# Performance work log

Measured on AMD Instinct MI355X. Metric: run time of the kernel, lower is better.

Reference implementation:

```python
import jax, jax.numpy as jnp
import numpy as np

IN_FEATURES = 1024
OUT_FEATURES = 1024
GRID_SIZE = 5
SPLINE_ORDER = 3
N_BASIS = GRID_SIZE + SPLINE_ORDER  # 8, matches spline_weight last dim
N_GRID = GRID_SIZE + 2 * SPLINE_ORDER + 1  # 12 knots -> Cox-de-Boor yields N_BASIS bases


def b_spline(x, grid):
    # x: [B, I] -> bases: [B, I, N_BASIS]
    x = x[..., None]
    bases = ((x >= grid[:-1]) & (x < grid[1:])).astype(x.dtype)
    for k in range(1, SPLINE_ORDER + 1):
        left = (x - grid[: -k - 1]) / (grid[k:-1] - grid[: -k - 1] + 1e-8)
        right = (grid[k + 1:] - x) / (grid[k + 1:] - grid[1:-k] + 1e-8)
        bases = left * bases[..., :-1] + right * bases[..., 1:]
    return bases


def setup_inputs() -> dict:
    key = jax.random.key(0)
    k1, k2, k3 = jax.random.split(key, 3)
    x = jax.random.uniform(k1, (4096, IN_FEATURES), dtype=jnp.float32) * 2.0 - 1.0
    # kaiming_uniform_(a=sqrt(5)) on [out,in]: bound = 1/sqrt(in)
    bound = 1.0 / np.sqrt(IN_FEATURES)
    base_weight = jax.random.uniform(k2, (OUT_FEATURES, IN_FEATURES), dtype=jnp.float32,
                                     minval=-bound, maxval=bound)
    spline_weight = 0.1 * jax.random.normal(k3, (OUT_FEATURES, IN_FEATURES, N_BASIS), dtype=jnp.float32)
    grid = jnp.linspace(-1.0, 1.0, N_GRID, dtype=jnp.float32)
    return {"x": x, "base_weight": base_weight, "spline_weight": spline_weight, "grid": grid}


def reference(x, base_weight, spline_weight, grid):
    base_output = jax.nn.silu(x) @ base_weight.T  # [B, O]
    spline_basis = b_spline(x, grid)              # [B, I, Q]
    spline_output = jnp.einsum('biq,oiq->bo', spline_basis, spline_weight)
    return base_output + spline_output
```

## Files before the change

### kernel.cpp

```cpp
#include <hip/hip_runtime.h>
#include <hip/hip_bf16.h>

#define IN_F 1024
#define OUT_F 1024
#define QP 9
#define KDIM (IN_F * QP)
#define SPLITK 2
#define KSLICE (KDIM / SPLITK)
#define BK 64

typedef __attribute__((ext_vector_type(8))) short short8;
typedef __attribute__((ext_vector_type(4))) float floatx4;
typedef __attribute__((ext_vector_type(8))) unsigned short ushort8v;

__device__ __forceinline__ unsigned short f2bf(float f) {
    union { float f; unsigned u; } v; v.f = f;
    return (unsigned short)((v.u + 0x7FFF + ((v.u >> 16) & 1)) >> 16);
}

__global__ __launch_bounds__(256) void pack_kernel(const float* __restrict__ x,
                                                   const float* __restrict__ bw,
                                                   const float* __restrict__ sw,
                                                   __hip_bfloat16* __restrict__ A,
                                                   __hip_bfloat16* __restrict__ W, int Bm) {
    const int nb_a = (Bm * IN_F / 8) / 256;
    if ((int)blockIdx.x < nb_a) {
        int t  = blockIdx.x * 256 + threadIdx.x;
        int b  = t >> 7;
        int i0 = (t & 127) * 8;
        const float4* xr = (const float4*)(x + (size_t)b * IN_F + i0);
        float4 x0 = xr[0], x1 = xr[1];
        float xv[8] = {x0.x, x0.y, x0.z, x0.w, x1.x, x1.y, x1.z, x1.w};
        ushort8v ov[9];
#pragma unroll
        for (int e = 0; e < 8; ++e) {
            float v  = xv[e];
            float u  = (v + 1.0f) * 5.5f;
            float fj = floorf(u);
            int   j  = (int)fj;
            float tt = u - fj;
            float t2 = tt * tt, t3 = t2 * tt;
            float omt = 1.0f - tt;
            float w0 = omt * omt * omt * (1.0f / 6.0f);
            float w1 = (3.0f * t3 - 6.0f * t2 + 4.0f) * (1.0f / 6.0f);
            float w2 = (-3.0f * t3 + 3.0f * t2 + 3.0f * tt + 1.0f) * (1.0f/6.0f);
            float w3 = t3 * (1.0f / 6.0f);
            ov[0][e] = f2bf(v * __builtin_amdgcn_rcpf(1.0f + __expf(-v)));
#pragma unroll
            for (int q = 0; q < 8; ++q) {
                int d = j - q;
                float bv = (d == 3) ? w0 : (d == 2) ? w1 : (d == 1) ? w2 : (d == 0) ? w3 : 0.0f;
                ov[1 + q][e] = f2bf(bv);
            }
        }
        unsigned short* dst = (unsigned short*)A + (size_t)b * KDIM + i0;
#pragma unroll
        for (int s = 0; s < QP; ++s)
            *(ushort8v*)(dst + (size_t)s * IN_F) = ov[s];
    } else {
        int t = ((int)blockIdx.x - nb_a) * 256 + threadIdx.x;
        unsigned short* dst = (unsigned short*)W + (size_t)(t >> 10) * KDIM + (t & 1023);
        dst[0] = f2bf(bw[t]);
        const float4* s4 = (const float4*)(sw + (size_t)t * 8);
        float4 lo = s4[0], hi = s4[1];
        dst[1 * IN_F] = f2bf(lo.x); dst[2 * IN_F] = f2bf(lo.y);
        dst[3 * IN_F] = f2bf(lo.z); dst[4 * IN_F] = f2bf(lo.w);
        dst[5 * IN_F] = f2bf(hi.x); dst[6 * IN_F] = f2bf(hi.y);
        dst[7 * IN_F] = f2bf(hi.z); dst[8 * IN_F] = f2bf(hi.w);
    }
}

__global__ __launch_bounds__(256, 2) void gemm_splitk(const __hip_bfloat16* __restrict__ A,
                                                      const __hip_bfloat16* __restrict__ W,
                                                      float* __restrict__ P, int Bm) {
    __shared__ short sA[128 * BK];
    __shared__ short sB[128 * BK];
    const int tid   = threadIdx.x;
    const int lane  = tid & 63;
    const int wave  = tid >> 6;
    const int row16 = lane & 15;
    const int quad  = lane >> 4;
    const int wm = wave >> 1, wn = wave & 1;
    const int m0 = blockIdx.y * 128;
    const int n0 = blockIdx.x * 128;
    const int kb = blockIdx.z * KSLICE;

    const short* Ag = (const short*)A + (size_t)m0 * KDIM + kb;
    const short* Wg = (const short*)W + (size_t)n0 * KDIM + kb;

    floatx4 acc[4][4] = {};

    int rs[4], ko[4], ld[4];
#pragma unroll
    for (int p = 0; p < 4; ++p) {
        int c = p * 256 + tid;
        rs[p] = c >> 3;
        ko[p] = (((c & 7) ^ ((rs[p] >> 1) & 7)) * 8);
        ld[p] = c * 8;
    }

    for (int k0 = 0; k0 < KSLICE; k0 += BK) {
#pragma unroll
        for (int p = 0; p < 4; ++p)
            __builtin_amdgcn_global_load_lds(
                (const __attribute__((address_space(1))) void*)(Ag + (size_t)rs[p] * KDIM + k0 + ko[p]),
                (__attribute__((address_space(3))) void*)(sA + ld[p]), 16, 0, 0);
#pragma unroll
        for (int p = 0; p < 4; ++p)
            __builtin_amdgcn_global_load_lds(
                (const __attribute__((address_space(1))) void*)(Wg + (size_t)rs[p] * KDIM + k0 + ko[p]),
                (__attribute__((address_space(3))) void*)(sB + ld[p]), 16, 0, 0);
        __syncthreads();

#pragma unroll
        for (int ks = 0; ks < 2; ++ks) {
            short8 aF[4], bF[4];
#pragma unroll
            for (int mi = 0; mi < 4; ++mi) {
                int r = wm * 64 + mi * 16 + row16;
                int pc = (ks * 4 + quad) ^ ((r >> 1) & 7);
                aF[mi] = *(const short8*)&sA[r * BK + pc * 8];
            }
#pragma unroll
            for (int ni = 0; ni < 4; ++ni) {
                int r = wn * 64 + ni * 16 + row16;
                int pc = (ks * 4 + quad) ^ ((r >> 1) & 7);
                bF[ni] = *(const short8*)&sB[r * BK + pc * 8];
            }
#pragma unroll
            for (int mi = 0; mi < 4; ++mi)
#pragma unroll
                for (int ni = 0; ni < 4; ++ni)
                    acc[mi][ni] = __builtin_amdgcn_mfma_f32_16x16x32_bf16(
                        aF[mi], bF[ni], acc[mi][ni], 0, 0, 0);
        }
        __syncthreads();
    }

    float* Pz = P + (size_t)blockIdx.z * Bm * OUT_F;
#pragma unroll
    for (int mi = 0; mi < 4; ++mi)
#pragma unroll
        for (int r = 0; r < 4; ++r) {
            int gm = m0 + wm * 64 + mi * 16 + quad * 4 + r;
            float* crow = Pz + (size_t)gm * OUT_F + n0 + wn * 64 + row16;
#pragma unroll
            for (int ni = 0; ni < 4; ++ni)
                crow[ni * 16] = acc[mi][ni][r];
        }
}

__global__ __launch_bounds__(256) void reduce_kernel(const float4* __restrict__ P,
                                                     float4* __restrict__ C, int n4) {
    int t = blockIdx.x * 256 + threadIdx.x;
    float4 a = P[t], b = P[n4 + t];
    float4 o;
    o.x = a.x + b.x; o.y = a.y + b.y; o.z = a.z + b.z; o.w = a.w + b.w;
    C[t] = o;
}

__global__ __launch_bounds__(256, 2) void gemm_kernel(const __hip_bfloat16* __restrict__ A,
                                                      const __hip_bfloat16* __restrict__ W,
                                                      float* __restrict__ C) {
    __shared__ short sA[128 * 32];
    __shared__ short sB[64 * 32];
    const int tid   = threadIdx.x;
    const int lane  = tid & 63;
    const int wave  = tid >> 6;
    const int row16 = lane & 15;
    const int quad  = lane >> 4;
    const int wm = wave >> 1, wn = wave & 1;
    const int m0 = blockIdx.y * 128;
    const int n0 = blockIdx.x * 64;
    const short* Ag = (const short*)A + (size_t)m0 * KDIM;
    const short* Wg = (const short*)W + (size_t)n0 * KDIM;
    floatx4 acc[4][2] = {};
    const int cA0 = tid,       rA0 = cA0 >> 2, kA0 = (((cA0 & 3) ^ ((rA0 >> 1) & 3)) * 8);
    const int cA1 = 256 + tid, rA1 = cA1 >> 2, kA1 = (((cA1 & 3) ^ ((rA1 >> 1) & 3)) * 8);
    const int cB  = tid,       rB  = cB  >> 2, kB  = (((cB  & 3) ^ ((rB  >> 1) & 3)) * 8);
    for (int k0 = 0; k0 < KDIM; k0 += 32) {
        __builtin_amdgcn_global_load_lds(
            (const __attribute__((address_space(1))) void*)(Ag + (size_t)rA0 * KDIM + k0 + kA0),
            (__attribute__((address_space(3))) void*)(sA + cA0 * 8), 16, 0, 0);
        __builtin_amdgcn_global_load_lds(
            (const __attribute__((address_space(1))) void*)(Ag + (size_t)rA1 * KDIM + k0 + kA1),
            (__attribute__((address_space(3))) void*)(sA + cA1 * 8), 16, 0, 0);
        __builtin_amdgcn_global_load_lds(
            (const __attribute__((address_space(1))) void*)(Wg + (size_t)rB * KDIM + k0 + kB),
            (__attribute__((address_space(3))) void*)(sB + cB * 8), 16, 0, 0);
        __syncthreads();
        short8 aF[4], bF[2];
#pragma unroll
        for (int mi = 0; mi < 4; ++mi) {
            int r = wm * 64 + mi * 16 + row16;
            aF[mi] = *(const short8*)&sA[r * 32 + ((quad ^ ((r >> 1) & 3)) * 8)];
        }
#pragma unroll
        for (int ni = 0; ni < 2; ++ni) {
            int r = wn * 32 + ni * 16 + row16;
            bF[ni] = *(const short8*)&sB[r * 32 + ((quad ^ ((r >> 1) & 3)) * 8)];
        }
#pragma unroll
        for (int mi = 0; mi < 4; ++mi)
#pragma unroll
            for (int ni = 0; ni < 2; ++ni)
                acc[mi][ni] = __builtin_amdgcn_mfma_f32_16x16x32_bf16(
                    aF[mi], bF[ni], acc[mi][ni], 0, 0, 0);
        __syncthreads();
    }
#pragma unroll
    for (int mi = 0; mi < 4; ++mi)
#pragma unroll
        for (int r = 0; r < 4; ++r) {
            int gm = m0 + wm * 64 + mi * 16 + quad * 4 + r;
            float* crow = C + (size_t)gm * OUT_F + n0 + wn * 32 + row16;
            crow[0]  = acc[mi][0][r];
            crow[16] = acc[mi][1][r];
        }
}

__global__ __launch_bounds__(256) void fallback_kernel(const float* __restrict__ x,
                                                       const float* __restrict__ bw,
                                                       const float* __restrict__ sw,
                                                       const float* __restrict__ grid,
                                                       float* __restrict__ out, int Bm) {
    __shared__ float sv[256][QP + 1];
    int b = blockIdx.y;
    int o = blockIdx.x * 256 + threadIdx.x;
    float acc = 0.f;
    for (int ic = 0; ic < IN_F; ic += 256) {
        int i = ic + threadIdx.x;
        float v = x[(size_t)b * IN_F + i];
        float g[12];
        for (int j = 0; j < 12; ++j) g[j] = grid[j];
        float bb[11];
        for (int j = 0; j < 11; ++j) bb[j] = (v >= g[j] && v < g[j + 1]) ? 1.f : 0.f;
        for (int k = 1; k <= 3; ++k)
            for (int j = 0; j < 11 - k; ++j)
                bb[j] = (v - g[j]) / (g[j + k] - g[j] + 1e-8f) * bb[j]
                      + (g[j + k + 1] - v) / (g[j + k + 1] - g[j + 1] + 1e-8f) * bb[j + 1];
        __syncthreads();
        sv[threadIdx.x][0] = v / (1.f + __expf(-v));
        for (int q = 0; q < 8; ++q) sv[threadIdx.x][1 + q] = bb[q];
        __syncthreads();
        for (int ii = 0; ii < 256; ++ii) {
            int i2 = ic + ii;
            acc += sv[ii][0] * bw[(size_t)o * IN_F + i2];
            const float* swp = sw + ((size_t)o * IN_F + i2) * 8;
            for (int q = 0; q < 8; ++q) acc += sv[ii][1 + q] * swp[q];
        }
    }
    out[(size_t)b * OUT_F + o] = acc;
}

extern "C" void kernel_launch(void* const* d_in, const int* in_sizes, int n_in,
                              void* d_out, int out_size, void* d_ws, size_t ws_size,
                              hipStream_t stream) {
    const float* x    = (const float*)d_in[0];
    const float* bw   = (const float*)d_in[1];
    const float* sw   = (const float*)d_in[2];
    const float* grid = (const float*)d_in[3];
    float* out = (float*)d_out;

    const int Bm = in_sizes[0] / IN_F;
    const size_t a_bytes = (size_t)Bm * KDIM * sizeof(__hip_bfloat16);
    const size_t w_bytes = (size_t)OUT_F * KDIM * sizeof(__hip_bfloat16);
    const size_t p_bytes = (size_t)SPLITK * Bm * OUT_F * sizeof(float);

    if (ws_size >= a_bytes + w_bytes && (Bm % 128) == 0) {
        __hip_bfloat16* Apk = (__hip_bfloat16*)d_ws;
        __hip_bfloat16* Wpk = (__hip_bfloat16*)((char*)d_ws + a_bytes);
        const int nb_a = (Bm * IN_F / 8) / 256;
        const int nb_w = (OUT_F * IN_F) / 256;
        pack_kernel<<<nb_a + nb_w, 256, 0, stream>>>(x, bw, sw, Apk, Wpk, Bm);
        if (ws_size >= a_bytes + w_bytes + p_bytes) {
            float* P = (float*)((char*)d_ws + a_bytes + w_bytes);
            gemm_splitk<<<dim3(OUT_F / 128, Bm / 128, SPLITK), 256, 0, stream>>>(Apk, Wpk, P, Bm);
            reduce_kernel<<<Bm * OUT_F / 1024, 256, 0, stream>>>((const float4*)P, (float4*)out,
                                                                 Bm * OUT_F / 4);
        } else {
            gemm_kernel<<<dim3(OUT_F / 64, Bm / 128), 256, 0, stream>>>(Apk, Wpk, out);
        }
    } else {
        fallback_kernel<<<dim3(OUT_F / 256, Bm), 256, 0, stream>>>(x, bw, sw, grid, out, Bm);
    }
}
```

Before: 218.1 us.

## Replace split-K partial buffer and reduce kernel with atomic accumulation into output

The split-K GEMM now zeroes the output with a memset and has each K-slice atomically add its tile into the final output, which removes the partial-sum buffer and the separate reduce kernel. The split factor goes from 2 to 4, giving 1024 blocks instead of 512. The non-split fallback GEMM is deleted. In exchange the output takes four-way float atomic traffic and a memset launch, and the summation order is no longer deterministic.

```diff
diff --git a/kernel.cpp b/kernel.cpp
--- a/kernel.cpp
+++ b/kernel.cpp
@@ -5,7 +5,7 @@
 #define OUT_F 1024
 #define QP 9
 #define KDIM (IN_F * QP)
-#define SPLITK 2
+#define SPLITK 4
 #define KSLICE (KDIM / SPLITK)
 #define BK 64
 
@@ -72,7 +72,7 @@
 
 __global__ __launch_bounds__(256, 2) void gemm_splitk(const __hip_bfloat16* __restrict__ A,
                                                       const __hip_bfloat16* __restrict__ W,
-                                                      float* __restrict__ P, int Bm) {
+                                                      float* __restrict__ C, int Bm) {
     __shared__ short sA[128 * BK];
     __shared__ short sB[128 * BK];
     const int tid   = threadIdx.x;
@@ -137,85 +137,15 @@
         __syncthreads();
     }
 
-    float* Pz = P + (size_t)blockIdx.z * Bm * OUT_F;
 #pragma unroll
     for (int mi = 0; mi < 4; ++mi)
 #pragma unroll
         for (int r = 0; r < 4; ++r) {
             int gm = m0 + wm * 64 + mi * 16 + quad * 4 + r;
-            float* crow = Pz + (size_t)gm * OUT_F + n0 + wn * 64 + row16;
+            float* crow = C + (size_t)gm * OUT_F + n0 + wn * 64 + row16;
 #pragma unroll
             for (int ni = 0; ni < 4; ++ni)
-                crow[ni * 16] = acc[mi][ni][r];
-        }
-}
-
-__global__ __launch_bounds__(256) void reduce_kernel(const float4* __restrict__ P,
-                                                     float4* __restrict__ C, int n4) {
-    int t = blockIdx.x * 256 + threadIdx.x;
-    float4 a = P[t], b = P[n4 + t];
-    float4 o;
-    o.x = a.x + b.x; o.y = a.y + b.y; o.z = a.z + b.z; o.w = a.w + b.w;
-    C[t] = o;
-}
-
-__global__ __launch_bounds__(256, 2) void gemm_kernel(const __hip_bfloat16* __restrict__ A,
-                                                      const __hip_bfloat16* __restrict__ W,
-                                                      float* __restrict__ C) {
-    __shared__ short sA[128 * 32];
-    __shared__ short sB[64 * 32];
-    const int tid   = threadIdx.x;
-    const int lane  = tid & 63;
-    const int wave  = tid >> 6;
-    const int row16 = lane & 15;
-    const int quad  = lane >> 4;
-    const int wm = wave >> 1, wn = wave & 1;
-    const int m0 = blockIdx.y * 128;
-    const int n0 = blockIdx.x * 64;
-    const short* Ag = (const short*)A + (size_t)m0 * KDIM;
-    const short* Wg = (const short*)W + (size_t)n0 * KDIM;
-    floatx4 acc[4][2] = {};
-    const int cA0 = tid,       rA0 = cA0 >> 2, kA0 = (((cA0 & 3) ^ ((rA0 >> 1) & 3)) * 8);
-    const int cA1 = 256 + tid, rA1 = cA1 >> 2, kA1 = (((cA1 & 3) ^ ((rA1 >> 1) & 3)) * 8);
-    const int cB  = tid,       rB  = cB  >> 2, kB  = (((cB  & 3) ^ ((rB  >> 1) & 3)) * 8);
-    for (int k0 = 0; k0 < KDIM; k0 += 32) {
-        __builtin_amdgcn_global_load_lds(
-            (const __attribute__((address_space(1))) void*)(Ag + (size_t)rA0 * KDIM + k0 + kA0),
-            (__attribute__((address_space(3))) void*)(sA + cA0 * 8), 16, 0, 0);
-        __builtin_amdgcn_global_load_lds(
-            (const __attribute__((address_space(1))) void*)(Ag + (size_t)rA1 * KDIM + k0 + kA1),
-            (__attribute__((address_space(3))) void*)(sA + cA1 * 8), 16, 0, 0);
-        __builtin_amdgcn_global_load_lds(
-            (const __attribute__((address_space(1))) void*)(Wg + (size_t)rB * KDIM + k0 + kB),
-            (__attribute__((address_space(3))) void*)(sB + cB * 8), 16, 0, 0);
-        __syncthreads();
-        short8 aF[4], bF[2];
-#pragma unroll
-        for (int mi = 0; mi < 4; ++mi) {
-            int r = wm * 64 + mi * 16 + row16;
-            aF[mi] = *(const short8*)&sA[r * 32 + ((quad ^ ((r >> 1) & 3)) * 8)];
-        }
-#pragma unroll
-        for (int ni = 0; ni < 2; ++ni) {
-            int r = wn * 32 + ni * 16 + row16;
-            bF[ni] = *(const short8*)&sB[r * 32 + ((quad ^ ((r >> 1) & 3)) * 8)];
-        }
-#pragma unroll
-        for (int mi = 0; mi < 4; ++mi)
-#pragma unroll
-            for (int ni = 0; ni < 2; ++ni)
-                acc[mi][ni] = __builtin_amdgcn_mfma_f32_16x16x32_bf16(
-                    aF[mi], bF[ni], acc[mi][ni], 0, 0, 0);
-        __syncthreads();
-    }
-#pragma unroll
-    for (int mi = 0; mi < 4; ++mi)
-#pragma unroll
-        for (int r = 0; r < 4; ++r) {
-            int gm = m0 + wm * 64 + mi * 16 + quad * 4 + r;
-            float* crow = C + (size_t)gm * OUT_F + n0 + wn * 32 + row16;
-            crow[0]  = acc[mi][0][r];
-            crow[16] = acc[mi][1][r];
+                unsafeAtomicAdd(&crow[ni * 16], acc[mi][ni][r]);
         }
 }
 
@@ -265,7 +195,6 @@
     const int Bm = in_sizes[0] / IN_F;
     const size_t a_bytes = (size_t)Bm * KDIM * sizeof(__hip_bfloat16);
     const size_t w_bytes = (size_t)OUT_F * KDIM * sizeof(__hip_bfloat16);
-    const size_t p_bytes = (size_t)SPLITK * Bm * OUT_F * sizeof(float);
 
     if (ws_size >= a_bytes + w_bytes && (Bm % 128) == 0) {
         __hip_bfloat16* Apk = (__hip_bfloat16*)d_ws;
@@ -273,14 +202,8 @@
         const int nb_a = (Bm * IN_F / 8) / 256;
         const int nb_w = (OUT_F * IN_F) / 256;
         pack_kernel<<<nb_a + nb_w, 256, 0, stream>>>(x, bw, sw, Apk, Wpk, Bm);
-        if (ws_size >= a_bytes + w_bytes + p_bytes) {
-            float* P = (float*)((char*)d_ws + a_bytes + w_bytes);
-            gemm_splitk<<<dim3(OUT_F / 128, Bm / 128, SPLITK), 256, 0, stream>>>(Apk, Wpk, P, Bm);
-            reduce_kernel<<<Bm * OUT_F / 1024, 256, 0, stream>>>((const float4*)P, (float4*)out,
-                                                                 Bm * OUT_F / 4);
-        } else {
-            gemm_kernel<<<dim3(OUT_F / 64, Bm / 128), 256, 0, stream>>>(Apk, Wpk, out);
-        }
+        hipMemsetAsync(out, 0, (size_t)Bm * OUT_F * sizeof(float), stream);
+        gemm_splitk<<<dim3(OUT_F / 128, Bm / 128, SPLITK), 256, 0, stream>>>(Apk, Wpk, out, Bm);
     } else {
         fallback_kernel<<<dim3(OUT_F / 256, Bm), 256, 0, stream>>>(x, bw, sw, grid, out, Bm);
     }
```

Measured after the change: 239.4 us. 9.8% more time.
